# Kernel optimization log

Hardware: AMD Instinct MI355X
Metric: run time of the kernel (lower is better)

The kernel has to match this reference:

```python
import jax, jax.numpy as jnp
import numpy as np

B, T, H, O = 256, 512, 1024, 256


def setup_inputs() -> dict:
    key = jax.random.key(0)
    k0, k1, k2, k3, k4 = jax.random.split(key, 5)
    scale_ih = 1.0 / np.sqrt(1 + H)
    scale_ho = 1.0 / np.sqrt(H)
    return {
        "x": jax.random.normal(k0, (B, T), dtype=jnp.float32),
        "W_ih": jax.random.normal(k1, (1 + H, H), dtype=jnp.float32) * scale_ih,
        "b_ih": jax.random.normal(k2, (H,), dtype=jnp.float32) * scale_ih,
        "W_ho": jax.random.normal(k3, (H, O), dtype=jnp.float32) * scale_ho,
        "b_ho": jax.random.normal(k4, (O,), dtype=jnp.float32) * scale_ho,
    }


def reference(x, W_ih, b_ih, W_ho, b_ho):
    # Elman RNN cell: hidden = tanh(W_ih @ [x_t; h]); output = W_ho @ h_T.
    # Only the final timestep's output is returned by the original module,
    # so h2o is applied once to the final hidden state (identical math).
    batch = x.shape[0]
    h0 = jnp.zeros((batch, W_ih.shape[1]), dtype=x.dtype)

    def step(h, x_t):  # x_t: [B], h: [B, H]
        combined = jnp.concatenate([x_t[:, None], h], axis=1)  # [B, 1+H]
        h_new = jnp.tanh(combined @ W_ih + b_ih)               # [B, H]
        return h_new, None

    h_final, _ = jax.lax.scan(step, h0, x.T)  # scan over T
    return h_final @ W_ho + b_ho              # [B, O]
```

## Files before the change

kernel.cpp:

```cpp
#include <hip/hip_runtime.h>
#include <hip/hip_bf16.h>


#define Bsz 256
#define Tn  512
#define Hn  1024
#define On  256

typedef __attribute__((ext_vector_type(8))) _Float16 f16x8;
typedef __attribute__((ext_vector_type(4))) float f32x4;
typedef __attribute__((ext_vector_type(4))) int   i32x4;
typedef __attribute__((ext_vector_type(2))) int   i32x2;

__device__ __forceinline__ unsigned f2h(float f) {
    _Float16 h = (_Float16)f;
    union { _Float16 h; unsigned short s; } u; u.h = h;
    return (unsigned)u.s;
}

__device__ __forceinline__ f16x8 as_f16x8(i32x4 v) {
    union { i32x4 i; f16x8 h; } u; u.i = v; return u.h;
}

__device__ __forceinline__ float fast_tanh(float x) {
    float xc = fminf(fmaxf(x, -9.f), 9.f);
    float e  = __builtin_amdgcn_exp2f(xc * 2.8853900817779268f);
    return (e - 1.f) * __builtin_amdgcn_rcpf(e + 1.f);
}

#define MFMA_F16 __builtin_amdgcn_mfma_f32_16x16x32_f16

__device__ __forceinline__ void stage_quarter(const short* __restrict__ hsrc,
                                              short* __restrict__ htile,
                                              int row0, int cg, int kq,
                                              int lane, unsigned tag) {
    const int half = lane >> 5, gl = lane & 31, r0 = cg * 8;
    const short* a0 = hsrc + (size_t)(row0 + r0 + 0 + half) * Hn + kq * 256 + gl * 8;
    const short* a1 = hsrc + (size_t)(row0 + r0 + 2 + half) * Hn + kq * 256 + gl * 8;
    const short* a2 = hsrc + (size_t)(row0 + r0 + 4 + half) * Hn + kq * 256 + gl * 8;
    const short* a3 = hsrc + (size_t)(row0 + r0 + 6 + half) * Hn + kq * 256 + gl * 8;
    i32x4 t0, t1, t2, t3;
    int spin = 0;
    for (;;) {
        asm volatile("global_load_dwordx4 %0, %1, off sc0 sc1"
                     : "=&v"(t0) : "v"(a0) : "memory");
        asm volatile("global_load_dwordx4 %0, %1, off sc0 sc1"
                     : "=&v"(t1) : "v"(a1) : "memory");
        asm volatile("global_load_dwordx4 %0, %1, off sc0 sc1"
                     : "=&v"(t2) : "v"(a2) : "memory");
        asm volatile("global_load_dwordx4 %0, %1, off sc0 sc1"
                     : "=&v"(t3) : "v"(a3) : "memory");
        asm volatile("s_waitcnt vmcnt(0)" ::: "memory");
        unsigned bad = 0;
#pragma unroll
        for (int e = 0; e < 4; ++e)
            bad |= (unsigned)(t0[e] ^ tag) | (unsigned)(t1[e] ^ tag) |
                   (unsigned)(t2[e] ^ tag) | (unsigned)(t3[e] ^ tag);
        if (!__any(bad & 1u)) break;
        if (++spin > (1 << 20)) break;
    }
    i32x4 tv[4] = {t0, t1, t2, t3};
#pragma unroll
    for (int p = 0; p < 4; ++p) {
        int row = r0 + 2 * p + half;
        int g   = kq * 32 + gl;
        int idx = row * 128 + (g ^ (row & 7));
        *(i32x4*)(htile + idx * 8) = tv[p];
    }
}

__global__ __launch_bounds__(512, 2) void rnn_kernel(
    const float* __restrict__ x,
    const float* __restrict__ W_ih,
    const float* __restrict__ b_ih,
    const float* __restrict__ W_ho,
    const float* __restrict__ b_ho,
    float* __restrict__ out,
    short* __restrict__ hbuf)
{
    const int tid  = threadIdx.x;
    const int lane = tid & 63;
    const int w    = tid >> 6;
    const int cg   = w >> 2;
    const int kq   = w & 3;
    const int q    = lane >> 4;
    const int n    = lane & 15;

    const int i = blockIdx.x & 15;
    const int j = blockIdx.x >> 4;
    const int colbase = j * 128 + cg * 64;
    const int owncol  = colbase + kq * 16 + 4 * q;
    const int row0    = i * 16;

    __shared__ float x_lds[16][Tn + 1];
    __shared__ short htile[16 * Hn];
    __shared__ float redbuf[2][8 * 3 * 256];
    __shared__ int   pairflag[4];

    if (tid < 4) pairflag[tid] = 0;

    for (int idx = tid; idx < 16 * Tn; idx += 512) {
        int r = idx >> 9, tt = idx & (Tn - 1);
        x_lds[r][tt] = x[(row0 + r) * Tn + tt];
    }

    f16x8 wfrag[32];
#pragma unroll
    for (int mt = 0; mt < 4; ++mt)
#pragma unroll
        for (int ks = 0; ks < 8; ++ks) {
#pragma unroll
            for (int e = 0; e < 8; ++e) {
                int k = kq * 256 + ks * 32 + q * 8 + e;
                wfrag[mt * 8 + ks][e] =
                    (_Float16)W_ih[(size_t)(1 + k) * Hn + colbase + mt * 16 + n];
            }
        }
    const float4 bias4 = *(const float4*)(b_ih + owncol);
    const float4 w04   = *(const float4*)(W_ih + owncol);

    __syncthreads();

    short* h0 = hbuf;
    short* h1 = hbuf + Bsz * Hn;
    const int swn   = n & 7;
    const int gbase = kq * 32;
    const int slot  = (q * 16 + n) * 4;
    const f32x4 zero4 = {0.f, 0.f, 0.f, 0.f};

    for (int t = 0; t < Tn; ++t) {
        const float xv = x_lds[n][t];
        f32x4 aown = {bias4.x + xv * w04.x, bias4.y + xv * w04.y,
                      bias4.z + xv * w04.z, bias4.w + xv * w04.w};
        f32x4 hv;

        if (t > 0) {
            stage_quarter((t & 1) ? h1 : h0, htile, row0, cg, kq, lane,
                          (unsigned)((t + 1) >> 1) & 1u);
            asm volatile("s_waitcnt lgkmcnt(0)" ::: "memory");
            if (lane == 0)
                __hip_atomic_fetch_add(&pairflag[kq], 1, __ATOMIC_RELAXED,
                                       __HIP_MEMORY_SCOPE_WORKGROUP);
            while (__hip_atomic_load(&pairflag[kq], __ATOMIC_RELAXED,
                                     __HIP_MEMORY_SCOPE_WORKGROUP) < 2 * t) {}
            asm volatile("" ::: "memory");

            f32x4 acc0 = (kq == 0) ? aown : zero4;
            f32x4 acc1 = (kq == 1) ? aown : zero4;
            f32x4 acc2 = (kq == 2) ? aown : zero4;
            f32x4 acc3 = (kq == 3) ? aown : zero4;
            const i32x4* lrow = (const i32x4*)(htile + n * Hn);
#pragma unroll
            for (int ks = 0; ks < 8; ++ks) {
                f16x8 b = as_f16x8(lrow[(gbase + ks * 4 + q) ^ swn]);
                acc0 = MFMA_F16(wfrag[0 * 8 + ks], b, acc0, 0, 0, 0);
                acc1 = MFMA_F16(wfrag[1 * 8 + ks], b, acc1, 0, 0, 0);
                acc2 = MFMA_F16(wfrag[2 * 8 + ks], b, acc2, 0, 0, 0);
                acc3 = MFMA_F16(wfrag[3 * 8 + ks], b, acc3, 0, 0, 0);
            }

            float* rb = redbuf[t & 1];
#define WRITE_PART(MT, ACC)                                                  \
            if (kq != MT) {                                                  \
                int src = (kq < MT) ? kq : kq - 1;                           \
                *(f32x4*)(rb + ((cg * 4 + MT) * 3 + src) * 256 + slot) = ACC;\
            }
            WRITE_PART(0, acc0)
            WRITE_PART(1, acc1)
            WRITE_PART(2, acc2)
            WRITE_PART(3, acc3)
#undef WRITE_PART
            __syncthreads();

            hv = (kq == 0) ? acc0 : (kq == 1) ? acc1 : (kq == 2) ? acc2 : acc3;
            const float* bp = rb + (cg * 4 + kq) * 3 * 256 + slot;
            f32x4 p0 = *(const f32x4*)(bp);
            f32x4 p1 = *(const f32x4*)(bp + 256);
            f32x4 p2 = *(const f32x4*)(bp + 512);
            hv = hv + p0 + p1 + p2;
        } else {
            hv = aown;
        }

        unsigned tagn = (unsigned)((t + 2) >> 1) & 1u;
        unsigned e0 = f2h(fast_tanh(hv[0])), e1 = f2h(fast_tanh(hv[1]));
        unsigned e2 = f2h(fast_tanh(hv[2])), e3 = f2h(fast_tanh(hv[3]));
        i32x2 pk;
        pk[0] = (int)(((e0 & ~1u) | tagn) | (e1 << 16));
        pk[1] = (int)(((e2 & ~1u) | tagn) | (e3 << 16));
        short* hdst = (((t + 1) & 1) ? h1 : h0) + (size_t)(row0 + n) * Hn + owncol;
        asm volatile("global_store_dwordx2 %0, %1, off sc0 sc1"
                     :: "v"(hdst), "v"(pk) : "memory");
        asm volatile("s_waitcnt vmcnt(0)" ::: "memory");
    }

    stage_quarter(h0, htile, row0, cg, kq, lane, 0u);
    __syncthreads();

    f32x4 e0 = zero4, e1 = zero4;
    {
        const i32x4* lrow = (const i32x4*)(htile + n * Hn);
#pragma unroll
        for (int kk = 0; kk < 4; ++kk) {
            f16x8 af = as_f16x8(lrow[(w * 16 + kk * 4 + q) ^ swn]);
            f16x8 b0, b1;
#pragma unroll
            for (int e = 0; e < 8; ++e) {
                const float* wp = W_ho +
                    (size_t)(w * 128 + kk * 32 + q * 8 + e) * On + j * 32 + n;
                b0[e] = (_Float16)wp[0];
                b1[e] = (_Float16)wp[16];
            }
            e0 = MFMA_F16(af, b0, e0, 0, 0, 0);
            e1 = MFMA_F16(af, b1, e1, 0, 0, 0);
        }
    }
    {
        float* re = redbuf[0] + w * 528;
#pragma unroll
        for (int r = 0; r < 4; ++r) {
            re[(4 * q + r) * 33 + n]      = e0[r];
            re[(4 * q + r) * 33 + 16 + n] = e1[r];
        }
    }
    __syncthreads();
    {
        int r = tid >> 5, c = tid & 31;
        float s = b_ho[j * 32 + c];
#pragma unroll
        for (int w8 = 0; w8 < 8; ++w8)
            s += redbuf[0][w8 * 528 + r * 33 + c];
        out[(size_t)(row0 + r) * On + j * 32 + c] = s;
    }
}

extern "C" void kernel_launch(void* const* d_in, const int* in_sizes, int n_in,
                              void* d_out, int out_size, void* d_ws, size_t ws_size,
                              hipStream_t stream) {
    const float* x    = (const float*)d_in[0];
    const float* W_ih = (const float*)d_in[1];
    const float* b_ih = (const float*)d_in[2];
    const float* W_ho = (const float*)d_in[3];
    const float* b_ho = (const float*)d_in[4];
    float* out = (float*)d_out;

    size_t need = (size_t)2 * Bsz * Hn * sizeof(short);
    if (ws_size < need) return;

    short* hbuf = (short*)d_ws;

    rnn_kernel<<<128, 512, 0, stream>>>(x, W_ih, b_ih, W_ho, b_ho, out, hbuf);
}
```

Measured before the change: 1.092 ms.

## Replace block-wide barrier with per-column-group LDS counters and drop store wait

```diff
diff --git a/kernel.cpp b/kernel.cpp
--- a/kernel.cpp
+++ b/kernel.cpp
@@ -30,10 +30,27 @@
 
 #define MFMA_F16 __builtin_amdgcn_mfma_f32_16x16x32_f16
 
+#define WG_SCOPE __HIP_MEMORY_SCOPE_WORKGROUP
+
+__device__ __forceinline__ void ctr_wait(int* ctr, int need) {
+    int guard = 0;
+    while (__hip_atomic_load(ctr, __ATOMIC_RELAXED, WG_SCOPE) < need) {
+        if (++guard > (1 << 22)) break;
+    }
+    asm volatile("" ::: "memory");
+}
+
+__device__ __forceinline__ void ctr_bump(int* ctr, int lane) {
+    asm volatile("s_waitcnt lgkmcnt(0)" ::: "memory");
+    if (lane == 0)
+        __hip_atomic_fetch_add(ctr, 1, __ATOMIC_RELAXED, WG_SCOPE);
+}
+
 __device__ __forceinline__ void stage_quarter(const short* __restrict__ hsrc,
                                               short* __restrict__ htile,
                                               int row0, int cg, int kq,
-                                              int lane, unsigned tag) {
+                                              int lane, unsigned tag,
+                                              int* consumed, int need) {
     const int half = lane >> 5, gl = lane & 31, r0 = cg * 8;
     const short* a0 = hsrc + (size_t)(row0 + r0 + 0 + half) * Hn + kq * 256 + gl * 8;
     const short* a1 = hsrc + (size_t)(row0 + r0 + 2 + half) * Hn + kq * 256 + gl * 8;
@@ -59,6 +76,7 @@
         if (!__any(bad & 1u)) break;
         if (++spin > (1 << 20)) break;
     }
+    ctr_wait(consumed, need);
     i32x4 tv[4] = {t0, t1, t2, t3};
 #pragma unroll
     for (int p = 0; p < 4; ++p) {
@@ -96,8 +114,11 @@
     __shared__ short htile[16 * Hn];
     __shared__ float redbuf[2][8 * 3 * 256];
     __shared__ int   pairflag[4];
-
-    if (tid < 4) pairflag[tid] = 0;
+    __shared__ int   pairdone[4];
+    __shared__ int   cgbar[2];
+
+    if (tid < 4) { pairflag[tid] = 0; pairdone[tid] = 0; }
+    if (tid < 2) cgbar[tid] = 0;
 
     for (int idx = tid; idx < 16 * Tn; idx += 512) {
         int r = idx >> 9, tt = idx & (Tn - 1);
@@ -136,14 +157,10 @@
 
         if (t > 0) {
             stage_quarter((t & 1) ? h1 : h0, htile, row0, cg, kq, lane,
-                          (unsigned)((t + 1) >> 1) & 1u);
-            asm volatile("s_waitcnt lgkmcnt(0)" ::: "memory");
-            if (lane == 0)
-                __hip_atomic_fetch_add(&pairflag[kq], 1, __ATOMIC_RELAXED,
-                                       __HIP_MEMORY_SCOPE_WORKGROUP);
-            while (__hip_atomic_load(&pairflag[kq], __ATOMIC_RELAXED,
-                                     __HIP_MEMORY_SCOPE_WORKGROUP) < 2 * t) {}
-            asm volatile("" ::: "memory");
+                          (unsigned)((t + 1) >> 1) & 1u,
+                          &pairdone[kq], 2 * (t - 1));
+            ctr_bump(&pairflag[kq], lane);
+            ctr_wait(&pairflag[kq], 2 * t);
 
             f32x4 acc0 = (kq == 0) ? aown : zero4;
             f32x4 acc1 = (kq == 1) ? aown : zero4;
@@ -158,7 +175,9 @@
                 acc2 = MFMA_F16(wfrag[2 * 8 + ks], b, acc2, 0, 0, 0);
                 acc3 = MFMA_F16(wfrag[3 * 8 + ks], b, acc3, 0, 0, 0);
             }
-
+            ctr_bump(&pairdone[kq], lane);
+
+            ctr_wait(&cgbar[cg], 4 * (t - 1));
             float* rb = redbuf[t & 1];
 #define WRITE_PART(MT, ACC)                                                  \
             if (kq != MT) {                                                  \
@@ -170,7 +189,8 @@
             WRITE_PART(2, acc2)
             WRITE_PART(3, acc3)
 #undef WRITE_PART
-            __syncthreads();
+            ctr_bump(&cgbar[cg], lane);
+            ctr_wait(&cgbar[cg], 4 * t);
 
             hv = (kq == 0) ? acc0 : (kq == 1) ? acc1 : (kq == 2) ? acc2 : acc3;
             const float* bp = rb + (cg * 4 + kq) * 3 * 256 + slot;
@@ -191,10 +211,10 @@
         short* hdst = (((t + 1) & 1) ? h1 : h0) + (size_t)(row0 + n) * Hn + owncol;
         asm volatile("global_store_dwordx2 %0, %1, off sc0 sc1"
                      :: "v"(hdst), "v"(pk) : "memory");
-        asm volatile("s_waitcnt vmcnt(0)" ::: "memory");
-    }
-
-    stage_quarter(h0, htile, row0, cg, kq, lane, 0u);
+    }
+
+    stage_quarter(h0, htile, row0, cg, kq, lane, 0u,
+                  &pairdone[kq], 2 * (Tn - 1));
     __syncthreads();
 
     f32x4 e0 = zero4, e1 = zero4;
```

Result: slower. 1.542 ms (+41.2%).
